# Optimization experiments

Hardware: AMD Instinct MI355X
Metric: run time of the kernel (lower is better)

The kernel has to match this reference:

```python
import jax, jax.numpy as jnp
import numpy as np

N_NODES, IN_FEAT, N_HEADS, N_HIDDEN = 4096, 1433, 8, 64
NEG_SLOPE = 0.2

def setup_inputs() -> dict:
    key = jax.random.key(0)
    k1, k2, k3 = jax.random.split(key, 3)
    vertex = jax.random.normal(k1, (N_NODES, IN_FEAT), dtype=jnp.float32)
    # linear_vert: Linear(in_features, n_hidden*n_heads, bias=False) -> weight [H*d, F]
    W_vert = jax.random.normal(k2, (N_HEADS * N_HIDDEN, IN_FEAT), dtype=jnp.float32) * (1.0 / np.sqrt(IN_FEAT))
    # attn: Linear(n_heads, n_heads, bias=False) -> weight [H, H]
    W_attn = jax.random.normal(k3, (N_HEADS, N_HEADS), dtype=jnp.float32) * (1.0 / np.sqrt(N_HEADS))
    return {"vertex": vertex, "W_vert": W_vert, "W_attn": W_attn}

def reference(vertex, W_vert, W_attn):
    n = vertex.shape[0]
    # g_vertex: [N, H, d]
    g = (vertex @ W_vert.T).reshape(n, N_HEADS, N_HIDDEN)
    # per-head Gram matrices, stacked on last dim: [N, N, H]
    gram = jnp.einsum('nhd,mhd->nmh', g, g)
    # head-mixing linear (H->H) + leaky relu, then sum over heads: [N, N]
    e = jax.nn.leaky_relu(jnp.einsum('nmh,gh->nmg', gram, W_attn), negative_slope=NEG_SLOPE)
    return e.sum(axis=-1)
```

## Files before the change

### kernel.cpp

```cpp
#include <hip/hip_runtime.h>
#include <hip/hip_bf16.h>

#define NN   4096
#define FIN  1433
#define KPAD 1536
#define NH   8
#define ND   64
#define CD   512

typedef float f32x4 __attribute__((ext_vector_type(4)));
typedef short s16x8 __attribute__((ext_vector_type(8)));

#define MFMA16(a, b, c) __builtin_amdgcn_mfma_f32_16x16x32_bf16((a), (b), (c), 0, 0, 0)

__device__ __forceinline__ void gload_lds16(const void* g, void* l) {
  __builtin_amdgcn_global_load_lds((const __attribute__((address_space(1))) void*)g,
                                   (__attribute__((address_space(3))) void*)l, 16, 0, 0);
}

__device__ __forceinline__ ushort f2bf(float x) {
  __hip_bfloat16 b = __float2bfloat16(x);
  ushort u;
  __builtin_memcpy(&u, &b, 2);
  return u;
}

__global__ void castpad_kernel(const float* __restrict__ src, ushort* __restrict__ dst,
                               int rows, int kin, int kout) {
  int i = blockIdx.x * blockDim.x + threadIdx.x;
  int kg = kout >> 3;
  int total = rows * kg;
  if (i >= total) return;
  int r  = i / kg;
  int k0 = (i - r * kg) << 3;
  s16x8 v;
#pragma unroll
  for (int j = 0; j < 8; ++j) {
    int k = k0 + j;
    float f = (k < kin) ? src[(size_t)r * kin + k] : 0.0f;
    v[j] = (short)f2bf(f);
  }
  *reinterpret_cast<s16x8*>(&dst[(size_t)r * kout + k0]) = v;
}

__global__ __launch_bounds__(256, 4) void gemm1_kernel(const ushort* __restrict__ A,
                                                       const ushort* __restrict__ B,
                                                       ushort* __restrict__ G) {
  __shared__ ushort As[2][64][64];
  __shared__ ushort Bs[2][64][64];
  const int tid  = threadIdx.x;
  const int lane = tid & 63;
  const int w    = tid >> 6;
  const int wr   = w >> 1, wc = w & 1;
  const int row0 = blockIdx.y * 64;
  const int col0 = blockIdx.x * 64;

  f32x4 acc[2][2] = {};

  auto stage = [&](int buf, int k0) {
#pragma unroll
    for (int c = 0; c < 2; ++c) {
      int ci = (w * 2 + c) * 64 + lane;
      int r  = ci >> 3;
      int cp = ci & 7;
      int gc = cp ^ (r & 7);
      gload_lds16(A + (size_t)(row0 + r) * KPAD + k0 + gc * 8,
                  &As[buf][0][0] + (size_t)(w * 2 + c) * 512);
      gload_lds16(B + (size_t)(col0 + r) * KPAD + k0 + gc * 8,
                  &Bs[buf][0][0] + (size_t)(w * 2 + c) * 512);
    }
  };

  stage(0, 0);
  __syncthreads();
  int cur = 0;

  for (int k0 = 0; k0 < KPAD; k0 += 64) {
    if (k0 + 64 < KPAD) stage(cur ^ 1, k0 + 64);
#pragma unroll
    for (int kk = 0; kk < 64; kk += 32) {
      int kq = (kk >> 3) + (lane >> 4);
      s16x8 af[2], bfv[2];
#pragma unroll
      for (int f = 0; f < 2; ++f) {
        int ar = wr * 32 + f * 16 + (lane & 15);
        af[f]  = *reinterpret_cast<const s16x8*>(&As[cur][ar][(kq ^ (ar & 7)) * 8]);
        int br = wc * 32 + f * 16 + (lane & 15);
        bfv[f] = *reinterpret_cast<const s16x8*>(&Bs[cur][br][(kq ^ (br & 7)) * 8]);
      }
#pragma unroll
      for (int fi = 0; fi < 2; ++fi)
#pragma unroll
        for (int fj = 0; fj < 2; ++fj)
          acc[fi][fj] = MFMA16(af[fi], bfv[fj], acc[fi][fj]);
    }
    __syncthreads();
    cur ^= 1;
  }

#pragma unroll
  for (int fi = 0; fi < 2; ++fi)
#pragma unroll
    for (int fj = 0; fj < 2; ++fj)
#pragma unroll
      for (int r = 0; r < 4; ++r) {
        int gr = row0 + wr * 32 + fi * 16 + (lane >> 4) * 4 + r;
        int gcol = col0 + wc * 32 + fj * 16 + (lane & 15);
        G[(size_t)gr * CD + gcol] = f2bf(acc[fi][fj][r]);
      }
}

__global__ __launch_bounds__(256, 2) void gram_kernel(const ushort* __restrict__ G,
                                                      const float* __restrict__ Wattn,
                                                      float* __restrict__ out) {
  const int bi = blockIdx.y;
  const int bj = blockIdx.x;
  if (bj < bi) return;

  __shared__ union LdsU {
    struct { ushort A[2][64][64]; ushort B[2][64][64]; } s;
    float t[64][65];
  } lds;
  __shared__ float sW[8][8];

  const int tid  = threadIdx.x;
  const int lane = tid & 63;
  const int w    = tid >> 6;
  const int wr   = w >> 1, wc = w & 1;
  const int ri0  = bi * 64, ci0 = bj * 64;

  if (tid < 64) sW[tid >> 3][tid & 7] = Wattn[tid];

  f32x4 acc[8][2][2] = {};

  auto stage = [&](int buf, int h) {
#pragma unroll
    for (int c = 0; c < 2; ++c) {
      int ci = (w * 2 + c) * 64 + lane;
      int r  = ci >> 3;
      int cp = ci & 7;
      int gc = cp ^ (r & 7);
      gload_lds16(G + (size_t)(ri0 + r) * CD + h * 64 + gc * 8,
                  &lds.s.A[buf][0][0] + (size_t)(w * 2 + c) * 512);
      gload_lds16(G + (size_t)(ci0 + r) * CD + h * 64 + gc * 8,
                  &lds.s.B[buf][0][0] + (size_t)(w * 2 + c) * 512);
    }
  };

  stage(0, 0);
  __syncthreads();
  int cur = 0;

#pragma unroll
  for (int h = 0; h < 8; ++h) {
    if (h + 1 < 8) stage(cur ^ 1, h + 1);
#pragma unroll
    for (int kk = 0; kk < 64; kk += 32) {
      int kq = (kk >> 3) + (lane >> 4);
      s16x8 af[2], bfv[2];
#pragma unroll
      for (int f = 0; f < 2; ++f) {
        int ar = wr * 32 + f * 16 + (lane & 15);
        af[f]  = *reinterpret_cast<const s16x8*>(&lds.s.A[cur][ar][(kq ^ (ar & 7)) * 8]);
        int br = wc * 32 + f * 16 + (lane & 15);
        bfv[f] = *reinterpret_cast<const s16x8*>(&lds.s.B[cur][br][(kq ^ (br & 7)) * 8]);
      }
#pragma unroll
      for (int fi = 0; fi < 2; ++fi)
#pragma unroll
        for (int fj = 0; fj < 2; ++fj)
          acc[h][fi][fj] = MFMA16(af[fi], bfv[fj], acc[h][fi][fj]);
    }
    __syncthreads();
    cur ^= 1;
  }

  float o[2][2][4] = {};
#pragma unroll
  for (int g = 0; g < 8; ++g) {
    float z[2][2][4] = {};
#pragma unroll
    for (int h = 0; h < 8; ++h) {
      float wgh = sW[g][h];
#pragma unroll
      for (int fi = 0; fi < 2; ++fi)
#pragma unroll
        for (int fj = 0; fj < 2; ++fj)
#pragma unroll
          for (int r = 0; r < 4; ++r)
            z[fi][fj][r] = fmaf(acc[h][fi][fj][r], wgh, z[fi][fj][r]);
    }
#pragma unroll
    for (int fi = 0; fi < 2; ++fi)
#pragma unroll
      for (int fj = 0; fj < 2; ++fj)
#pragma unroll
        for (int r = 0; r < 4; ++r) {
          float zz = z[fi][fj][r];
          o[fi][fj][r] += fmaxf(zz, 0.2f * zz);
        }
  }

#pragma unroll
  for (int fi = 0; fi < 2; ++fi)
#pragma unroll
    for (int fj = 0; fj < 2; ++fj)
#pragma unroll
      for (int r = 0; r < 4; ++r) {
        int rr = wr * 32 + fi * 16 + (lane >> 4) * 4 + r;
        int cc = wc * 32 + fj * 16 + (lane & 15);
        out[(size_t)(ri0 + rr) * NN + ci0 + cc] = o[fi][fj][r];
      }

  if (bi != bj) {
    __syncthreads();
#pragma unroll
    for (int fi = 0; fi < 2; ++fi)
#pragma unroll
      for (int fj = 0; fj < 2; ++fj)
#pragma unroll
        for (int r = 0; r < 4; ++r) {
          int rr = wr * 32 + fi * 16 + (lane >> 4) * 4 + r;
          int cc = wc * 32 + fj * 16 + (lane & 15);
          lds.t[cc][rr] = o[fi][fj][r];
        }
    __syncthreads();
    int a  = tid >> 2;
    int cb = (tid & 3) * 16;
#pragma unroll
    for (int jj = 0; jj < 4; ++jj) {
      float4 v;
      v.x = lds.t[a][cb + jj * 4 + 0];
      v.y = lds.t[a][cb + jj * 4 + 1];
      v.z = lds.t[a][cb + jj * 4 + 2];
      v.w = lds.t[a][cb + jj * 4 + 3];
      *reinterpret_cast<float4*>(&out[(size_t)(ci0 + a) * NN + ri0 + cb + jj * 4]) = v;
    }
  }
}

extern "C" void kernel_launch(void* const* d_in, const int* in_sizes, int n_in,
                              void* d_out, int out_size, void* d_ws, size_t ws_size,
                              hipStream_t stream) {
  const float* vertex = (const float*)d_in[0];
  const float* Wvert  = (const float*)d_in[1];
  const float* Wattn  = (const float*)d_in[2];
  float* out = (float*)d_out;

  char* ws = (char*)d_ws;
  ushort* Va = (ushort*)ws;
  ushort* Wb = (ushort*)(ws + (size_t)NN * KPAD * 2);
  ushort* G  = (ushort*)(ws + (size_t)NN * KPAD * 2 + (size_t)CD * KPAD * 2);

  int tot1 = NN * (KPAD / 8);
  castpad_kernel<<<(tot1 + 255) / 256, 256, 0, stream>>>(vertex, Va, NN, FIN, KPAD);
  int tot2 = CD * (KPAD / 8);
  castpad_kernel<<<(tot2 + 255) / 256, 256, 0, stream>>>(Wvert, Wb, CD, FIN, KPAD);

  gemm1_kernel<<<dim3(CD / 64, NN / 64), 256, 0, stream>>>(Va, Wb, G);

  gram_kernel<<<dim3(NN / 64, NN / 64), 256, 0, stream>>>(G, Wattn, out);
}
```

Baseline: 204.8 us.

## Launch only upper-triangle gram tiles, deepen K staging, widen GEMM1 K-tile

```diff
diff --git a/kernel.cpp b/kernel.cpp
--- a/kernel.cpp
+++ b/kernel.cpp
@@ -43,11 +43,11 @@
   *reinterpret_cast<s16x8*>(&dst[(size_t)r * kout + k0]) = v;
 }
 
-__global__ __launch_bounds__(256, 4) void gemm1_kernel(const ushort* __restrict__ A,
+__global__ __launch_bounds__(256, 2) void gemm1_kernel(const ushort* __restrict__ A,
                                                        const ushort* __restrict__ B,
                                                        ushort* __restrict__ G) {
-  __shared__ ushort As[2][64][64];
-  __shared__ ushort Bs[2][64][64];
+  __shared__ ushort As[2][64][128];
+  __shared__ ushort Bs[2][64][128];
   const int tid  = threadIdx.x;
   const int lane = tid & 63;
   const int w    = tid >> 6;
@@ -59,15 +59,15 @@
 
   auto stage = [&](int buf, int k0) {
 #pragma unroll
-    for (int c = 0; c < 2; ++c) {
-      int ci = (w * 2 + c) * 64 + lane;
-      int r  = ci >> 3;
-      int cp = ci & 7;
+    for (int j = 0; j < 4; ++j) {
+      int ci = (w * 4 + j) * 64 + lane;
+      int r  = ci >> 4;
+      int cp = ci & 15;
       int gc = cp ^ (r & 7);
       gload_lds16(A + (size_t)(row0 + r) * KPAD + k0 + gc * 8,
-                  &As[buf][0][0] + (size_t)(w * 2 + c) * 512);
+                  &As[buf][0][0] + (size_t)(w * 4 + j) * 512);
       gload_lds16(B + (size_t)(col0 + r) * KPAD + k0 + gc * 8,
-                  &Bs[buf][0][0] + (size_t)(w * 2 + c) * 512);
+                  &Bs[buf][0][0] + (size_t)(w * 4 + j) * 512);
     }
   };
 
@@ -75,11 +75,11 @@
   __syncthreads();
   int cur = 0;
 
-  for (int k0 = 0; k0 < KPAD; k0 += 64) {
-    if (k0 + 64 < KPAD) stage(cur ^ 1, k0 + 64);
-#pragma unroll
-    for (int kk = 0; kk < 64; kk += 32) {
-      int kq = (kk >> 3) + (lane >> 4);
+  for (int k0 = 0; k0 < KPAD; k0 += 128) {
+    if (k0 + 128 < KPAD) stage(cur ^ 1, k0 + 128);
+#pragma unroll
+    for (int kk = 0; kk < 4; ++kk) {
+      int kq = kk * 4 + (lane >> 4);
       s16x8 af[2], bfv[2];
 #pragma unroll
       for (int f = 0; f < 2; ++f) {
@@ -113,12 +113,18 @@
 __global__ __launch_bounds__(256, 2) void gram_kernel(const ushort* __restrict__ G,
                                                       const float* __restrict__ Wattn,
                                                       float* __restrict__ out) {
-  const int bi = blockIdx.y;
-  const int bj = blockIdx.x;
-  if (bj < bi) return;
+  const int nwg = (NN / 64) * (NN / 64 + 1) / 2;
+  const int cpx = nwg / 8;
+  int b = blockIdx.x;
+  int t = (b % 8) * cpx + (b / 8);
+  int bi = (int)((129.0f - sqrtf(16641.0f - 8.0f * (float)t)) * 0.5f);
+  while ((129 * (bi + 1) - (bi + 1) * (bi + 1)) / 2 <= t) ++bi;
+  while ((129 * bi - bi * bi) / 2 > t) --bi;
+  const int bj = bi + (t - (129 * bi - bi * bi) / 2);
+  const int ri0 = bi * 64, ci0 = bj * 64;
 
   __shared__ union LdsU {
-    struct { ushort A[2][64][64]; ushort B[2][64][64]; } s;
+    struct { ushort A[64][256]; ushort B[64][256]; } s;
     float t[64][65];
   } lds;
   __shared__ float sW[8][8];
@@ -127,53 +133,58 @@
   const int lane = tid & 63;
   const int w    = tid >> 6;
   const int wr   = w >> 1, wc = w & 1;
-  const int ri0  = bi * 64, ci0 = bj * 64;
 
   if (tid < 64) sW[tid >> 3][tid & 7] = Wattn[tid];
 
   f32x4 acc[8][2][2] = {};
 
-  auto stage = [&](int buf, int h) {
-#pragma unroll
-    for (int c = 0; c < 2; ++c) {
-      int ci = (w * 2 + c) * 64 + lane;
-      int r  = ci >> 3;
-      int cp = ci & 7;
+  auto stage = [&](int p) {
+#pragma unroll
+    for (int j = 0; j < 8; ++j) {
+      int ci = (w * 8 + j) * 64 + lane;
+      int r  = ci >> 5;
+      int cp = ci & 31;
       int gc = cp ^ (r & 7);
-      gload_lds16(G + (size_t)(ri0 + r) * CD + h * 64 + gc * 8,
-                  &lds.s.A[buf][0][0] + (size_t)(w * 2 + c) * 512);
-      gload_lds16(G + (size_t)(ci0 + r) * CD + h * 64 + gc * 8,
-                  &lds.s.B[buf][0][0] + (size_t)(w * 2 + c) * 512);
+      gload_lds16(G + (size_t)(ri0 + r) * CD + p * 256 + gc * 8,
+                  &lds.s.A[0][0] + (size_t)(w * 8 + j) * 512);
+      gload_lds16(G + (size_t)(ci0 + r) * CD + p * 256 + gc * 8,
+                  &lds.s.B[0][0] + (size_t)(w * 8 + j) * 512);
     }
   };
 
-  stage(0, 0);
-  __syncthreads();
-  int cur = 0;
-
-#pragma unroll
-  for (int h = 0; h < 8; ++h) {
-    if (h + 1 < 8) stage(cur ^ 1, h + 1);
-#pragma unroll
-    for (int kk = 0; kk < 64; kk += 32) {
-      int kq = (kk >> 3) + (lane >> 4);
-      s16x8 af[2], bfv[2];
-#pragma unroll
-      for (int f = 0; f < 2; ++f) {
-        int ar = wr * 32 + f * 16 + (lane & 15);
-        af[f]  = *reinterpret_cast<const s16x8*>(&lds.s.A[cur][ar][(kq ^ (ar & 7)) * 8]);
-        int br = wc * 32 + f * 16 + (lane & 15);
-        bfv[f] = *reinterpret_cast<const s16x8*>(&lds.s.B[cur][br][(kq ^ (br & 7)) * 8]);
-      }
-#pragma unroll
-      for (int fi = 0; fi < 2; ++fi)
-#pragma unroll
-        for (int fj = 0; fj < 2; ++fj)
-          acc[h][fi][fj] = MFMA16(af[fi], bfv[fj], acc[h][fi][fj]);
-    }
-    __syncthreads();
-    cur ^= 1;
-  }
+  auto compute = [&](int p) {
+#pragma unroll
+    for (int hh = 0; hh < 4; ++hh) {
+#pragma unroll
+      for (int kk = 0; kk < 2; ++kk) {
+        int kq = kk * 4 + (lane >> 4);
+        s16x8 af[2], bfv[2];
+#pragma unroll
+        for (int f = 0; f < 2; ++f) {
+          int ar = wr * 32 + f * 16 + (lane & 15);
+          af[f]  = *reinterpret_cast<const s16x8*>(
+                     &lds.s.A[ar][((hh * 8 + kq) ^ (ar & 7)) * 8]);
+          int br = wc * 32 + f * 16 + (lane & 15);
+          bfv[f] = *reinterpret_cast<const s16x8*>(
+                     &lds.s.B[br][((hh * 8 + kq) ^ (br & 7)) * 8]);
+        }
+        int h = p * 4 + hh;
+#pragma unroll
+        for (int fi = 0; fi < 2; ++fi)
+#pragma unroll
+          for (int fj = 0; fj < 2; ++fj)
+            acc[h][fi][fj] = MFMA16(af[fi], bfv[fj], acc[h][fi][fj]);
+      }
+    }
+  };
+
+  stage(0);
+  __syncthreads();
+  compute(0);
+  __syncthreads();
+  stage(1);
+  __syncthreads();
+  compute(1);
 
   float o[2][2][4] = {};
 #pragma unroll
@@ -259,5 +270,6 @@
 
   gemm1_kernel<<<dim3(CD / 64, NN / 64), 256, 0, stream>>>(Va, Wb, G);
 
-  gram_kernel<<<dim3(NN / 64, NN / 64), 256, 0, stream>>>(G, Wattn, out);
-}
+  int ntri = (NN / 64) * (NN / 64 + 1) / 2;
+  gram_kernel<<<ntri, 256, 0, stream>>>(G, Wattn, out);
+}
```

Result: faster. 193.1 us (-5.7%).
